# Kernel tuning notes

Hardware: AMD Instinct MI355X
Metric: run time of the kernel (lower is better)

Reference implementation:

```python
import jax, jax.numpy as jnp
import numpy as np

FORGET_BIAS = 1.0  # TF BasicLSTMCell default


def setup_inputs() -> dict:
    key = jax.random.key(0)
    k1, k2, k3 = jax.random.split(key, 3)
    B, T, D, H = 64, 2048, 256, 256
    x = jax.random.normal(k1, (B, T, D), dtype=jnp.float32)
    # kernel initialized by tf.random_uniform_initializer(-0.1, 0.1)
    W = jax.random.uniform(k2, (D + H, 4 * H), dtype=jnp.float32, minval=-0.1, maxval=0.1)
    b = jnp.zeros((4 * H,), dtype=jnp.float32)
    seq_len = jax.random.randint(k3, (B,), 1, T + 1, dtype=jnp.int32)
    return {"x": x, "W": W, "b": b, "seq_len": seq_len}


def reference(x, W, b, seq_len):
    """tf.nn.dynamic_rnn over a BasicLSTMCell with sequence_length masking.

    x: [B, T, D], W: [D+H, 4H], b: [4H], seq_len: [B]
    Returns all outputs [B, T, H] (return_last=False, return_seq_2d=False).
    """
    B, T, D = x.shape
    H = W.shape[1] // 4
    xt = jnp.transpose(x, (1, 0, 2))  # [T, B, D] for time-major scan
    c0 = jnp.zeros((B, H), dtype=x.dtype)
    h0 = jnp.zeros((B, H), dtype=x.dtype)

    def step(carry, xb):
        c, h, t = carry
        gates = jnp.concatenate([xb, h], axis=1) @ W + b  # [B, 4H]
        i, j, f, o = jnp.split(gates, 4, axis=1)          # TF order: i, j(=g), f, o
        nc = c * jax.nn.sigmoid(f + FORGET_BIAS) + jax.nn.sigmoid(i) * jnp.tanh(j)
        nh = jnp.tanh(nc) * jax.nn.sigmoid(o)
        valid = (t < seq_len)[:, None]                    # dynamic_rnn masking
        c_next = jnp.where(valid, nc, c)
        h_next = jnp.where(valid, nh, h)
        y = jnp.where(valid, nh, jnp.zeros_like(nh))      # zero outputs past length
        return (c_next, h_next, t + 1), y

    (_, _, _), ys = jax.lax.scan(step, (c0, h0, jnp.int32(0)), xt)
    return jnp.transpose(ys, (1, 0, 2))  # [B, T, H]
```

## Files before the change

### kernel.cpp

```cpp
#include <hip/hip_runtime.h>
#include <hip/hip_fp16.h>
#include <cstdint>
#include <cstddef>

#define BB 64
#define TT 2048
#define DD 256
#define HH 256
#define G4 1024

typedef unsigned int u32;

__device__ __forceinline__ float sigf(float x) {
    return 1.0f / (1.0f + __expf(-x));
}
__device__ __forceinline__ float tanhfast(float x) {
    float ax = fabsf(x);
    float t  = __expf(-2.0f * ax);
    float r  = (1.0f - t) / (1.0f + t);
    return copysignf(r, x);
}

#if defined(__has_builtin)
#if __has_builtin(__builtin_amdgcn_fdot2)
#define HAVE_FDOT2 1
#endif
#endif

typedef _Float16 f16x2 __attribute__((ext_vector_type(2)));

__device__ __forceinline__ float dot2f(u32 a, u32 b, float c) {
#ifdef HAVE_FDOT2
    return __builtin_amdgcn_fdot2(__builtin_bit_cast(f16x2, a),
                                  __builtin_bit_cast(f16x2, b), c, false);
#else
    __half2 ah = *reinterpret_cast<__half2*>(&a);
    __half2 bh = *reinterpret_cast<__half2*>(&b);
    float2 af = __half22float2(ah), bf = __half22float2(bh);
    return c + af.x * bf.x + af.y * bf.y;
#endif
}

__global__ __launch_bounds__(256) void prep_wh(const float* __restrict__ W, u32* __restrict__ whp) {
    int idx = blockIdx.x * 256 + threadIdx.x;
    int k2 = idx >> 10, c = idx & 1023;
    float lo = W[(size_t)(DD + 2 * k2) * G4 + c];
    float hi = W[(size_t)(DD + 2 * k2 + 1) * G4 + c];
    __half2 h = __floats2half2_rn(lo, hi);
    whp[idx] = *reinterpret_cast<u32*>(&h);
}

__global__ __launch_bounds__(256) void init_state(float* __restrict__ cst, float* __restrict__ hst) {
    int i = blockIdx.x * 256 + threadIdx.x;
    cst[i] = 0.0f;
    hst[i] = 0.0f;
}

#define BM 128
#define BN 64
#define BK 32

__global__ __launch_bounds__(256) void gemm_xw(const float* __restrict__ x,
                                               const float* __restrict__ W,
                                               const float* __restrict__ bias,
                                               const int* __restrict__ seqlen,
                                               float* __restrict__ xw,
                                               int t0, int ct) {
    const int m0 = blockIdx.x * BM;
    const int b  = m0 / ct;
    const int tl0 = m0 - b * ct;
    if (t0 + tl0 >= seqlen[b]) return;
    const int n0 = blockIdx.y * BN;

    __shared__ __align__(16) float xs[BK][BM + 4];
    __shared__ __align__(16) float wsm[BK][BN];

    const int tid = threadIdx.x;
    const int tx = tid & 15, ty = tid >> 4;
    const float* xrowbase = x + ((size_t)b * TT + t0 + tl0) * DD;

    float4 acc[8];
    #pragma unroll
    for (int i = 0; i < 8; ++i) acc[i] = make_float4(0.f, 0.f, 0.f, 0.f);

    for (int k0 = 0; k0 < DD; k0 += BK) {
        #pragma unroll
        for (int i = 0; i < 4; ++i) {
            int idx = tid + i * 256;
            int r = idx >> 3, kv = idx & 7;
            float4 v = *reinterpret_cast<const float4*>(xrowbase + (size_t)r * DD + k0 + kv * 4);
            xs[kv * 4 + 0][r] = v.x; xs[kv * 4 + 1][r] = v.y;
            xs[kv * 4 + 2][r] = v.z; xs[kv * 4 + 3][r] = v.w;
        }
        #pragma unroll
        for (int i = 0; i < 2; ++i) {
            int idx = tid + i * 256;
            int kr = idx >> 4, cv = idx & 15;
            *reinterpret_cast<float4*>(&wsm[kr][cv * 4]) =
                *reinterpret_cast<const float4*>(W + (size_t)(k0 + kr) * G4 + n0 + cv * 4);
        }
        __syncthreads();
        #pragma unroll
        for (int k = 0; k < BK; ++k) {
            float4 a0 = *reinterpret_cast<const float4*>(&xs[k][ty * 8]);
            float4 a1 = *reinterpret_cast<const float4*>(&xs[k][ty * 8 + 4]);
            float4 bv = *reinterpret_cast<const float4*>(&wsm[k][tx * 4]);
            float ai[8] = {a0.x, a0.y, a0.z, a0.w, a1.x, a1.y, a1.z, a1.w};
            #pragma unroll
            for (int i = 0; i < 8; ++i) {
                acc[i].x += ai[i] * bv.x; acc[i].y += ai[i] * bv.y;
                acc[i].z += ai[i] * bv.z; acc[i].w += ai[i] * bv.w;
            }
        }
        __syncthreads();
    }
    float4 bv = *reinterpret_cast<const float4*>(bias + n0 + tx * 4);
    float* outbase = xw + (size_t)m0 * G4 + n0 + tx * 4;
    #pragma unroll
    for (int i = 0; i < 8; ++i) {
        float4 o = make_float4(acc[i].x + bv.x, acc[i].y + bv.y,
                               acc[i].z + bv.z, acc[i].w + bv.w);
        *reinterpret_cast<float4*>(outbase + (size_t)(ty * 8 + i) * G4) = o;
    }
}

#define NT 512
#define KREG 96
#define KLDS 32

__global__ __launch_bounds__(NT, 2) void lstm_chunk(const u32* __restrict__ whp,
                                                    const float* __restrict__ xw,
                                                    const int* __restrict__ seqlen,
                                                    float* __restrict__ y,
                                                    float* __restrict__ cst,
                                                    float* __restrict__ hst,
                                                    int t0, int ct) {
    __shared__ __align__(16) u32 w2lds[KLDS * 1024];
    __shared__ __align__(16) float g_sh[G4];
    __shared__ __align__(16) u32 h_sh_u[128];

    const int tid = threadIdx.x;
    const int b   = blockIdx.x;
    const int slen = seqlen[b];

    uint2 wr[KREG];
    #pragma unroll
    for (int i = 0; i < KREG; ++i)
        wr[i] = *reinterpret_cast<const uint2*>(whp + (size_t)i * 1024 + 2 * tid);

    {
        const uint4* src = reinterpret_cast<const uint4*>(whp + KREG * 1024);
        uint4* dst = reinterpret_cast<uint4*>(w2lds);
        for (int i = tid; i < (KLDS * 1024) / 4; i += NT) dst[i] = src[i];
    }

    __half* hs = reinterpret_cast<__half*>(h_sh_u);
    float c_r = 0.0f;
    if (tid < HH) {
        c_r = cst[b * HH + tid];
        hs[tid] = __float2half(hst[b * HH + tid]);
    }
    __syncthreads();

    const float* xwbase = xw + (size_t)b * ct * G4 + 2 * tid;
    float2 xwcur = *reinterpret_cast<const float2*>(xwbase);
    const uint4* h4 = reinterpret_cast<const uint4*>(h_sh_u);

    int tl = 0;
    for (; tl < ct; ++tl) {
        if (t0 + tl >= slen) break;

        float2 xwnext = xwcur;
        if (tl + 1 < ct)
            xwnext = *reinterpret_cast<const float2*>(xwbase + (size_t)(tl + 1) * G4);

        float a0 = xwcur.x, a1 = xwcur.y;

        #pragma unroll
        for (int kb = 0; kb < KREG / 4; ++kb) {
            uint4 hh = h4[kb];
            a0 = dot2f(hh.x, wr[4 * kb + 0].x, a0); a1 = dot2f(hh.x, wr[4 * kb + 0].y, a1);
            a0 = dot2f(hh.y, wr[4 * kb + 1].x, a0); a1 = dot2f(hh.y, wr[4 * kb + 1].y, a1);
            a0 = dot2f(hh.z, wr[4 * kb + 2].x, a0); a1 = dot2f(hh.z, wr[4 * kb + 2].y, a1);
            a0 = dot2f(hh.w, wr[4 * kb + 3].x, a0); a1 = dot2f(hh.w, wr[4 * kb + 3].y, a1);
        }
        #pragma unroll
        for (int kb = KREG / 4; kb < 32; ++kb) {
            uint4 hh = h4[kb];
            #pragma unroll
            for (int j = 0; j < 4; ++j) {
                int row = 4 * kb + j - KREG;
                uint2 wl = *reinterpret_cast<const uint2*>(&w2lds[row * 1024 + 2 * tid]);
                u32 hj = (j == 0) ? hh.x : (j == 1) ? hh.y : (j == 2) ? hh.z : hh.w;
                a0 = dot2f(hj, wl.x, a0);
                a1 = dot2f(hj, wl.y, a1);
            }
        }

        *reinterpret_cast<float2*>(&g_sh[2 * tid]) = make_float2(a0, a1);
        __syncthreads();

        if (tid < HH) {
            float gi = g_sh[tid];
            float gj = g_sh[HH + tid];
            float gf = g_sh[2 * HH + tid];
            float go = g_sh[3 * HH + tid];
            float nc = c_r * sigf(gf + 1.0f) + sigf(gi) * tanhfast(gj);
            float nh = tanhfast(nc) * sigf(go);
            c_r = nc;
            hs[tid] = __float2half(nh);
            y[((size_t)b * TT + t0 + tl) * HH + tid] = nh;
        }
        __syncthreads();
        xwcur = xwnext;
    }

    if (tl < ct) {
        float4 z = make_float4(0.f, 0.f, 0.f, 0.f);
        size_t base = ((size_t)b * TT + t0 + tl) * HH;
        size_t total = (size_t)(ct - tl) * HH;
        for (size_t i = 4 * (size_t)tid; i < total; i += 4 * NT)
            *reinterpret_cast<float4*>(y + base + i) = z;
    }

    if (tid < HH) {
        cst[b * HH + tid] = c_r;
        hst[b * HH + tid] = __half2float(hs[tid]);
    }
}

extern "C" void kernel_launch(void* const* d_in, const int* in_sizes, int n_in,
                              void* d_out, int out_size, void* d_ws, size_t ws_size,
                              hipStream_t stream) {
    (void)in_sizes; (void)n_in; (void)out_size;
    const float* x      = (const float*)d_in[0];
    const float* W      = (const float*)d_in[1];
    const float* bias   = (const float*)d_in[2];
    const int*   seqlen = (const int*)d_in[3];
    float* y = (float*)d_out;

    u32*   whp = (u32*)d_ws;
    float* cst = (float*)((char*)d_ws + (512 << 10));
    float* hst = cst + BB * HH;
    float* xwbuf = (float*)((char*)d_ws + (640 << 10));

    long long avail = (long long)ws_size - (640 << 10);
    int ctu = 128;
    if (avail > 0) {
        long long mx = avail / ((long long)BB * G4 * 4);
        int mm = (int)((mx / 128) * 128);
        if (mm >= 128) ctu = mm;
    }
    if (ctu > TT) ctu = TT;

    prep_wh<<<dim3(512), 256, 0, stream>>>(W, whp);
    init_state<<<dim3(64), 256, 0, stream>>>(cst, hst);

    int done = 0;
    while (done < TT) {
        int ct = ctu;
        if (ct > TT - done) ct = TT - done;
        gemm_xw<<<dim3((BB * ct) / BM, G4 / BN), 256, 0, stream>>>(x, W, bias, seqlen, xwbuf, done, ct);
        lstm_chunk<<<dim3(BB), NT, 0, stream>>>(whp, xwbuf, seqlen, y, cst, hst, done, ct);
        done += ct;
    }
}
```

Measured before the change: 5.297 ms.

## Keep all recurrent weights in registers and exchange gates via wave shuffles

The LSTM recurrence kernel now holds all 128 packed weight rows in registers (launch bounds drop to one block per CU) instead of splitting them between registers and LDS. Gate columns are remapped so each wave holds the i/j/f/o gates for the same hidden units, and lanes exchange them with xor shuffles rather than a shared-memory gate buffer. The h vector is double-buffered, so only one barrier per timestep is needed, and the dot product uses two accumulator chains for more ILP. In exchange, register pressure rises sharply with a risk of spills, and only a quarter of the lanes do the activation work.

Measured after the change: 9.802 ms. 1.85x slower.

```diff
diff --git a/kernel.cpp b/kernel.cpp
--- a/kernel.cpp
+++ b/kernel.cpp
@@ -125,94 +125,85 @@
 }
 
 #define NT 512
-#define KREG 96
-#define KLDS 32
-
-__global__ __launch_bounds__(NT, 2) void lstm_chunk(const u32* __restrict__ whp,
+#define KREG 128
+
+__global__ __launch_bounds__(NT, 1) void lstm_chunk(const u32* __restrict__ whp,
                                                     const float* __restrict__ xw,
                                                     const int* __restrict__ seqlen,
                                                     float* __restrict__ y,
                                                     float* __restrict__ cst,
                                                     float* __restrict__ hst,
                                                     int t0, int ct) {
-    __shared__ __align__(16) u32 w2lds[KLDS * 1024];
-    __shared__ __align__(16) float g_sh[G4];
-    __shared__ __align__(16) u32 h_sh_u[128];
+    __shared__ __align__(16) u32 hbuf[2][128];
 
     const int tid = threadIdx.x;
     const int b   = blockIdx.x;
     const int slen = seqlen[b];
+    const int w = tid >> 6;
+    const int l = tid & 63;
+    const int g = (l >> 4) & 3;
+    const int p = (l & 15) + 16 * w;
+    const int n0 = 256 * g + 2 * p;
 
     uint2 wr[KREG];
     #pragma unroll
     for (int i = 0; i < KREG; ++i)
-        wr[i] = *reinterpret_cast<const uint2*>(whp + (size_t)i * 1024 + 2 * tid);
-
-    {
-        const uint4* src = reinterpret_cast<const uint4*>(whp + KREG * 1024);
-        uint4* dst = reinterpret_cast<uint4*>(w2lds);
-        for (int i = tid; i < (KLDS * 1024) / 4; i += NT) dst[i] = src[i];
-    }
-
-    __half* hs = reinterpret_cast<__half*>(h_sh_u);
-    float c_r = 0.0f;
-    if (tid < HH) {
-        c_r = cst[b * HH + tid];
-        hs[tid] = __float2half(hst[b * HH + tid]);
+        wr[i] = *reinterpret_cast<const uint2*>(whp + (size_t)i * 1024 + n0);
+
+    const bool actlane = (l < 16);
+    float2 c01 = make_float2(0.f, 0.f);
+    if (actlane) {
+        c01 = *reinterpret_cast<const float2*>(cst + b * HH + 2 * p);
+        float2 h01 = *reinterpret_cast<const float2*>(hst + b * HH + 2 * p);
+        __half2 hp = __floats2half2_rn(h01.x, h01.y);
+        hbuf[0][p] = *reinterpret_cast<u32*>(&hp);
     }
     __syncthreads();
 
-    const float* xwbase = xw + (size_t)b * ct * G4 + 2 * tid;
-    float2 xwcur = *reinterpret_cast<const float2*>(xwbase);
-    const uint4* h4 = reinterpret_cast<const uint4*>(h_sh_u);
+    const float* xwbase = xw + ((size_t)b * ct) * G4 + n0;
+    float2 xwc = *reinterpret_cast<const float2*>(xwbase);
+    int pp = 0;
 
     int tl = 0;
     for (; tl < ct; ++tl) {
         if (t0 + tl >= slen) break;
 
-        float2 xwnext = xwcur;
+        float2 xwn = xwc;
         if (tl + 1 < ct)
-            xwnext = *reinterpret_cast<const float2*>(xwbase + (size_t)(tl + 1) * G4);
-
-        float a0 = xwcur.x, a1 = xwcur.y;
-
-        #pragma unroll
-        for (int kb = 0; kb < KREG / 4; ++kb) {
+            xwn = *reinterpret_cast<const float2*>(xwbase + (size_t)(tl + 1) * G4);
+
+        float a0 = xwc.x, a1 = xwc.y;
+        float e0 = 0.f, e1 = 0.f;
+
+        const uint4* h4 = reinterpret_cast<const uint4*>(hbuf[pp]);
+        #pragma unroll
+        for (int kb = 0; kb < 32; ++kb) {
             uint4 hh = h4[kb];
             a0 = dot2f(hh.x, wr[4 * kb + 0].x, a0); a1 = dot2f(hh.x, wr[4 * kb + 0].y, a1);
-            a0 = dot2f(hh.y, wr[4 * kb + 1].x, a0); a1 = dot2f(hh.y, wr[4 * kb + 1].y, a1);
+            e0 = dot2f(hh.y, wr[4 * kb + 1].x, e0); e1 = dot2f(hh.y, wr[4 * kb + 1].y, e1);
             a0 = dot2f(hh.z, wr[4 * kb + 2].x, a0); a1 = dot2f(hh.z, wr[4 * kb + 2].y, a1);
-            a0 = dot2f(hh.w, wr[4 * kb + 3].x, a0); a1 = dot2f(hh.w, wr[4 * kb + 3].y, a1);
-        }
-        #pragma unroll
-        for (int kb = KREG / 4; kb < 32; ++kb) {
-            uint4 hh = h4[kb];
-            #pragma unroll
-            for (int j = 0; j < 4; ++j) {
-                int row = 4 * kb + j - KREG;
-                uint2 wl = *reinterpret_cast<const uint2*>(&w2lds[row * 1024 + 2 * tid]);
-                u32 hj = (j == 0) ? hh.x : (j == 1) ? hh.y : (j == 2) ? hh.z : hh.w;
-                a0 = dot2f(hj, wl.x, a0);
-                a1 = dot2f(hj, wl.y, a1);
-            }
-        }
-
-        *reinterpret_cast<float2*>(&g_sh[2 * tid]) = make_float2(a0, a1);
+            e0 = dot2f(hh.w, wr[4 * kb + 3].x, e0); e1 = dot2f(hh.w, wr[4 * kb + 3].y, e1);
+        }
+        a0 += e0; a1 += e1;
+
+        float j0 = __shfl_xor(a0, 16), j1 = __shfl_xor(a1, 16);
+        float f0 = __shfl_xor(a0, 32), f1 = __shfl_xor(a1, 32);
+        float o0 = __shfl_xor(a0, 48), o1 = __shfl_xor(a1, 48);
+
+        if (actlane) {
+            float nc0 = c01.x * sigf(f0 + 1.0f) + sigf(a0) * tanhfast(j0);
+            float nc1 = c01.y * sigf(f1 + 1.0f) + sigf(a1) * tanhfast(j1);
+            float nh0 = tanhfast(nc0) * sigf(o0);
+            float nh1 = tanhfast(nc1) * sigf(o1);
+            c01 = make_float2(nc0, nc1);
+            __half2 hp = __floats2half2_rn(nh0, nh1);
+            hbuf[pp ^ 1][p] = *reinterpret_cast<u32*>(&hp);
+            *reinterpret_cast<float2*>(y + ((size_t)b * TT + t0 + tl) * HH + 2 * p) =
+                make_float2(nh0, nh1);
+        }
         __syncthreads();
-
-        if (tid < HH) {
-            float gi = g_sh[tid];
-            float gj = g_sh[HH + tid];
-            float gf = g_sh[2 * HH + tid];
-            float go = g_sh[3 * HH + tid];
-            float nc = c_r * sigf(gf + 1.0f) + sigf(gi) * tanhfast(gj);
-            float nh = tanhfast(nc) * sigf(go);
-            c_r = nc;
-            hs[tid] = __float2half(nh);
-            y[((size_t)b * TT + t0 + tl) * HH + tid] = nh;
-        }
-        __syncthreads();
-        xwcur = xwnext;
+        pp ^= 1;
+        xwc = xwn;
     }
 
     if (tl < ct) {
@@ -223,9 +214,12 @@
             *reinterpret_cast<float4*>(y + base + i) = z;
     }
 
-    if (tid < HH) {
-        cst[b * HH + tid] = c_r;
-        hst[b * HH + tid] = __half2float(hs[tid]);
+    if (actlane) {
+        *reinterpret_cast<float2*>(cst + b * HH + 2 * p) = c01;
+        u32 hu = hbuf[pp][p];
+        __half2 hp = *reinterpret_cast<__half2*>(&hu);
+        float2 hf = __half22float2(hp);
+        *reinterpret_cast<float2*>(hst + b * HH + 2 * p) = hf;
     }
 }
 
```
